# Performance work log

Measured on AMD Instinct MI355X. Metric: run time of the kernel, lower is better.

## Reference

```python
import jax, jax.numpy as jnp
import numpy as np

WS, OWS, NH = 16, 24, 2          # window size, overlap window size (=int(16*0.5)+16), num heads
PAD = (OWS - WS) // 2            # unfold padding = 4


def conv2d(x, w, b):
    kh, kw = w.shape[2], w.shape[3]
    out = jax.lax.conv_general_dilated(x, w, (1, 1), [(kh // 2, kh // 2), (kw // 2, kw // 2)],
                                       dimension_numbers=('NCHW', 'OIHW', 'NCHW'))
    return out + b[None, :, None, None]


def layer_norm(x, g, b, eps=1e-5):
    m = x.mean(-1, keepdims=True)
    v = ((x - m) ** 2).mean(-1, keepdims=True)
    return (x - m) * jax.lax.rsqrt(v + eps) * g + b


def stem(depth, cw1, cb1, cw2, cb2, cw3, cb3, cw4, cb4, in_g, in_b):
    # BasicConv(1->8,k3,relu) -> (8->16,k1,relu) -> (16->16,k3,relu) -> (16->32,k1) -> InstanceNorm2d(32,affine)
    y = jax.nn.relu(conv2d(depth, cw1, cb1))
    y = jax.nn.relu(conv2d(y, cw2, cb2))
    y = jax.nn.relu(conv2d(y, cw3, cb3))
    y = conv2d(y, cw4, cb4)
    m = y.mean((2, 3), keepdims=True)
    v = ((y - m) ** 2).mean((2, 3), keepdims=True)
    return (y - m) * jax.lax.rsqrt(v + 1e-5) * in_g[None, :, None, None] + in_b[None, :, None, None]


def ocab(xq, ykv, rpi, n1g, n1b, wq, bq, wkv, bkv, rpb, wp, bp, n2g, n2b, mw1, mb1, mw2, mb2):
    # Overlapping cross-attention block (HAT-style OCAB, cross variant: q from xq, kv from ykv).
    b, c, h, w = xq.shape
    x = xq.transpose(0, 2, 3, 1)   # b h w c
    y = ykv.transpose(0, 2, 3, 1)
    shortcut = x
    q = layer_norm(x, n1g, n1b) @ wq + bq          # b h w c
    kv = layer_norm(y, n1g, n1b) @ wkv + bkv       # b h w 2c
    nhw, nww = h // WS, w // WS
    # non-overlapping query windows: (b*nw, WS*WS, c)
    qw = q.reshape(b, nhw, WS, nww, WS, c).transpose(0, 1, 3, 2, 4, 5).reshape(b * nhw * nww, WS * WS, c)
    # overlapping kv windows via unfold (patch channel order = (channel, kh, kw), same as torch unfold)
    patches = jax.lax.conv_general_dilated_patches(kv.transpose(0, 3, 1, 2), (OWS, OWS), (WS, WS),
                                                   [(PAD, PAD), (PAD, PAD)])  # b, 2c*OWS*OWS, nhw, nww
    patches = patches.reshape(b, 2, c, OWS * OWS, nhw * nww).transpose(1, 0, 4, 3, 2).reshape(2, b * nhw * nww, OWS * OWS, c)
    k, v = patches[0], patches[1]
    d = c // NH
    qh = qw.reshape(-1, WS * WS, NH, d).transpose(0, 2, 1, 3) * (d ** -0.5)
    kh = k.reshape(-1, OWS * OWS, NH, d).transpose(0, 2, 1, 3)
    vh = v.reshape(-1, OWS * OWS, NH, d).transpose(0, 2, 1, 3)
    attn = jnp.einsum('whqd,whkd->whqk', qh, kh)
    attn = attn + rpb[rpi].transpose(2, 0, 1)[None]  # rel-pos bias -> [1, NH, WS*WS, OWS*OWS]
    attn = jax.nn.softmax(attn, axis=-1)
    out = jnp.einsum('whqk,whkd->whqd', attn, vh).transpose(0, 2, 1, 3).reshape(-1, WS * WS, c)
    # window reverse
    out = out.reshape(b, nhw, nww, WS, WS, c).transpose(0, 1, 3, 2, 4, 5).reshape(b, h, w, c)
    out = out @ wp + bp + shortcut
    out = out + (jax.nn.gelu(layer_norm(out, n2g, n2b) @ mw1 + mb1) @ mw2 + mb2)  # mlp_ratio=2
    return out.transpose(0, 3, 1, 2)


def setup_inputs():
    key = jax.random.key(0)
    ks = jax.random.split(key, 16)
    B, C, H, W = 1, 32, 256, 256
    s = 0.05
    return dict(
        x=jax.random.normal(ks[0], (B, C, H, W), jnp.float32),
        depth=jax.random.normal(ks[1], (B, 1, H, W), jnp.float32),
        rpi=jax.random.randint(ks[2], (WS * WS, OWS * OWS), 0, (WS + OWS - 1) ** 2),
        cw1=jax.random.normal(ks[3], (8, 1, 3, 3)) * s, cb1=jnp.zeros(8),
        cw2=jax.random.normal(ks[4], (16, 8, 1, 1)) * s, cb2=jnp.zeros(16),
        cw3=jax.random.normal(ks[5], (16, 16, 3, 3)) * s, cb3=jnp.zeros(16),
        cw4=jax.random.normal(ks[6], (32, 16, 1, 1)) * s, cb4=jnp.zeros(32),
        in_g=jnp.ones(32), in_b=jnp.zeros(32),
        n1g=jnp.ones(C), n1b=jnp.zeros(C),
        wq=jax.random.normal(ks[7], (C, C)) * s, bq=jnp.zeros(C),
        wkv=jax.random.normal(ks[8], (C, 2 * C)) * s, bkv=jnp.zeros(2 * C),
        rpb=jax.random.normal(ks[9], ((WS + OWS - 1) ** 2, NH)) * 0.02,
        wp=jax.random.normal(ks[10], (C, C)) * s, bp=jnp.zeros(C),
        n2g=jnp.ones(C), n2b=jnp.zeros(C),
        mw1=jax.random.normal(ks[11], (C, 2 * C)) * s, mb1=jnp.zeros(2 * C),
        mw2=jax.random.normal(ks[12], (2 * C, C)) * s, mb2=jnp.zeros(C),
    )


def reference(x, depth, rpi, cw1, cb1, cw2, cb2, cw3, cb3, cw4, cb4, in_g, in_b,
              n1g, n1b, wq, bq, wkv, bkv, rpb, wp, bp, n2g, n2b, mw1, mb1, mw2, mb2):
    f = stem(depth, cw1, cb1, cw2, cb2, cw3, cb3, cw4, cb4, in_g, in_b)
    a = (n1g, n1b, wq, bq, wkv, bkv, rpb, wp, bp, n2g, n2b, mw1, mb1, mw2, mb2)
    out1 = ocab(x, f, rpi, *a)   # shared OCAB weights, called twice with swapped roles
    out2 = ocab(f, x, rpi, *a)
    return out1 + out2 + x
```

## Files before the change

### kernel.cpp

```cpp
#include <hip/hip_runtime.h>
#include <hip/hip_bf16.h>

#define HW 65536
#define KPAD 584

typedef __attribute__((ext_vector_type(8))) short bf8;
typedef __attribute__((ext_vector_type(4))) float f4;

__device__ __forceinline__ unsigned short f2b(float x) {
  unsigned int u = __float_as_uint(x);
  unsigned int r = (u + 0x7fff + ((u >> 16) & 1)) >> 16;
  return (unsigned short)r;
}
__device__ __forceinline__ unsigned int pk2(float lo, float hi) {
  return (__float_as_uint(hi) & 0xffff0000u) | (__float_as_uint(lo) >> 16);
}
__device__ __forceinline__ float ex2(float x) { return __builtin_amdgcn_exp2f(x); }

__device__ __forceinline__ void stem_front_body(
    int bx, int t, const float* __restrict__ depth,
    const float* __restrict__ cw1, const float* __restrict__ cb1,
    const float* __restrict__ cw2, const float* __restrict__ cb2,
    float* __restrict__ t2) {
  int p = bx * 256 + t;
  int y = p >> 8, x = p & 255;
  float in9[9];
#pragma unroll
  for (int ky = 0; ky < 3; ky++)
#pragma unroll
    for (int kx = 0; kx < 3; kx++) {
      int yy = y + ky - 1, xx = x + kx - 1;
      bool ok = ((unsigned)yy < 256u) && ((unsigned)xx < 256u);
      in9[ky*3+kx] = ok ? depth[yy*256+xx] : 0.f;
    }
  float t1[8];
#pragma unroll
  for (int o = 0; o < 8; o++) {
    float s = cb1[o];
#pragma unroll
    for (int i = 0; i < 9; i++) s += in9[i] * cw1[o*9+i];
    t1[o] = fmaxf(s, 0.f);
  }
#pragma unroll
  for (int o = 0; o < 16; o++) {
    float s = cb2[o];
#pragma unroll
    for (int ci = 0; ci < 8; ci++) s += t1[ci] * cw2[o*8+ci];
    t2[o*HW + p] = fmaxf(s, 0.f);
  }
}

__device__ __forceinline__ void bias_body(
    int bx, int t, const int* __restrict__ rpi,
    const float* __restrict__ rpb, float* __restrict__ biasT) {
  int idx = bx*256 + t;
  int hd = idx / 147456;
  int rem = idx - hd*147456;
  int qt = rem / 9216;
  int r2 = rem - qt*9216;
  int kb = r2 >> 6;
  int q16 = (r2 >> 2) & 15;
  int r = r2 & 3;
  int key = kb*4 + r;
  int qq = qt*16 + q16;
  biasT[idx] = (rpb[rpi[qq*576 + key]*2 + hd] - 8.0f) * 1.44269504f;
}

__device__ __forceinline__ void lnmm16_body(
    int role, int bx, int t,
    float* ws, float* gs, float* bs, float* b2s, float* as, float* bbs,
    const float* __restrict__ x, const float* __restrict__ t4,
    const float* __restrict__ part,
    const float* __restrict__ ig, const float* __restrict__ ib,
    const float* __restrict__ n1g, const float* __restrict__ n1b,
    const float* __restrict__ wq, const float* __restrict__ bq,
    const float* __restrict__ wkv, const float* __restrict__ bkv,
    float* q1, float* kv1, float* q2, float* kv2) {
  const float *src, *wm, *bo; float* dst;
  int wstride, wcol; bool ain;
  if (role < 6) { src = x;  ain = false; } else { src = t4; ain = true; }
  switch (role) {
    default:
    case 0:  wm=wq;  wstride=32; wcol=0;  bo=bq;  dst=q1;               break;
    case 1:  wm=wq;  wstride=32; wcol=16; bo=bq;  dst=q1+16*HW;         break;
    case 2: case 3: case 4: case 5:
             wm=wkv; wstride=64; wcol=16*(role-2); bo=bkv; dst=kv2+16*(role-2)*HW; break;
    case 6:  wm=wq;  wstride=32; wcol=0;  bo=bq;  dst=q2;               break;
    case 7:  wm=wq;  wstride=32; wcol=16; bo=bq;  dst=q2+16*HW;         break;
    case 8: case 9: case 10: case 11:
             wm=wkv; wstride=64; wcol=16*(role-8); bo=bkv; dst=kv1+16*(role-8)*HW; break;
  }
  for (int i = t; i < 512; i += 256) ws[i] = wm[(i>>4)*wstride + wcol + (i&15)];
  if (t < 16) b2s[t] = bo[wcol + t];
  if (t < 32) {
    gs[t] = n1g[t]; bs[t] = n1b[t];
    if (ain) {
      float s = 0.f, ss = 0.f;
#pragma unroll
      for (int k = 0; k < 16; k++) { s += part[t*16+k]; ss += part[512 + t*16+k]; }
      float m = s * (1.f/65536.f);
      float var = ss * (1.f/65536.f) - m*m;
      float a = rsqrtf(var + 1e-5f) * ig[t];
      as[t] = a; bbs[t] = ib[t] - m*a;
    }
  }
  __syncthreads();
  int p = bx*256 + t;
  float v[32]; float s = 0.f;
  if (ain) {
#pragma unroll
    for (int c = 0; c < 32; c++) { v[c] = src[c*HW+p]*as[c] + bbs[c]; s += v[c]; }
  } else {
#pragma unroll
    for (int c = 0; c < 32; c++) { v[c] = src[c*HW+p]; s += v[c]; }
  }
  float m = s * 0.03125f;
  float ss = 0.f;
#pragma unroll
  for (int c = 0; c < 32; c++) { float d = v[c]-m; ss += d*d; }
  float rs = rsqrtf(ss*0.03125f + 1e-5f);
  float acc[16];
#pragma unroll
  for (int j = 0; j < 16; j++) acc[j] = b2s[j];
#pragma unroll
  for (int c = 0; c < 32; c++) {
    float ln = (v[c]-m)*rs*gs[c] + bs[c];
    const float4* w4 = (const float4*)&ws[c*16];
#pragma unroll
    for (int j4 = 0; j4 < 4; j4++) {
      float4 w = w4[j4];
      acc[j4*4+0] += ln*w.x; acc[j4*4+1] += ln*w.y;
      acc[j4*4+2] += ln*w.z; acc[j4*4+3] += ln*w.w;
    }
  }
#pragma unroll
  for (int j = 0; j < 16; j++) dst[j*HW+p] = acc[j];
}

__global__ __launch_bounds__(256) void k_misc(
    const float* __restrict__ depth,
    const float* __restrict__ cw1, const float* __restrict__ cb1,
    const float* __restrict__ cw2, const float* __restrict__ cb2,
    float* __restrict__ t2,
    const int* __restrict__ rpi, const float* __restrict__ rpb, float* __restrict__ biasT,
    const float* __restrict__ x, const float* __restrict__ t4, const float* __restrict__ part,
    const float* __restrict__ ig, const float* __restrict__ ib,
    const float* __restrict__ n1g, const float* __restrict__ n1b,
    const float* __restrict__ wq, const float* __restrict__ bq,
    const float* __restrict__ wkv, const float* __restrict__ bkv,
    float* q1, float* kv1, float* q2, float* kv2) {
  __shared__ __align__(16) float ws[512];
  __shared__ float gs[32], bs[32], b2s[16], as[32], bbs[32];
  int id = blockIdx.x, t = threadIdx.x;
  if (id < 256) { stem_front_body(id, t, depth, cw1, cb1, cw2, cb2, t2); return; }
  if (id < 1408) { bias_body(id - 256, t, rpi, rpb, biasT); return; }
  int r = id - 1408;
  lnmm16_body(r >> 8, r & 255, t, ws, gs, bs, b2s, as, bbs,
              x, t4, part, ig, ib, n1g, n1b, wq, bq, wkv, bkv, q1, kv1, q2, kv2);
}

__global__ __launch_bounds__(256) void k_lnmmB(
    const float* __restrict__ x, const float* __restrict__ t4, const float* __restrict__ part,
    const float* __restrict__ ig, const float* __restrict__ ib,
    const float* __restrict__ n1g, const float* __restrict__ n1b,
    const float* __restrict__ wq, const float* __restrict__ bq,
    const float* __restrict__ wkv, const float* __restrict__ bkv,
    float* q1, float* kv1, float* q2, float* kv2, int ybase) {
  __shared__ __align__(16) float ws[512];
  __shared__ float gs[32], bs[32], b2s[16], as[32], bbs[32];
  lnmm16_body(ybase + blockIdx.y, blockIdx.x, threadIdx.x, ws, gs, bs, b2s, as, bbs,
              x, t4, part, ig, ib, n1g, n1b, wq, bq, wkv, bkv, q1, kv1, q2, kv2);
}

__global__ __launch_bounds__(256) void k_conv3(
    const float* __restrict__ t2, const float* __restrict__ cw3,
    const float* __restrict__ cb3, float* __restrict__ t3) {
  int t = threadIdx.x;
  int p = blockIdx.x*256 + t;
  int og = blockIdx.y;
  int y = p >> 8, x = p & 255;
  float acc[4];
#pragma unroll
  for (int o = 0; o < 4; o++) acc[o] = cb3[og*4+o];
#pragma unroll 1
  for (int tap = 0; tap < 9; tap++) {
    int ky = tap/3 - 1, kx = tap - (tap/3)*3 - 1;
    int yy = y+ky, xx = x+kx;
    bool ok = ((unsigned)yy < 256u) && ((unsigned)xx < 256u);
    int pp = yy*256+xx;
#pragma unroll
    for (int ci = 0; ci < 16; ci++) {
      float v = ok ? t2[ci*HW+pp] : 0.f;
#pragma unroll
      for (int o = 0; o < 4; o++)
        acc[o] += v * cw3[(og*4+o)*144 + ci*9 + tap];
    }
  }
#pragma unroll
  for (int o = 0; o < 4; o++) t3[(og*4+o)*HW+p] = fmaxf(acc[o], 0.f);
}

__global__ __launch_bounds__(256) void k_conv4(
    const float* __restrict__ t3, const float* __restrict__ cw4,
    const float* __restrict__ cb4, float* __restrict__ t4) {
  int t = threadIdx.x;
  int p = blockIdx.x*256 + t;
  int og = blockIdx.y;
  float v[16];
#pragma unroll
  for (int ci = 0; ci < 16; ci++) v[ci] = t3[ci*HW+p];
#pragma unroll
  for (int o = 0; o < 8; o++) {
    int oo = og*8 + o;
    float s = cb4[oo];
#pragma unroll
    for (int ci = 0; ci < 16; ci++) s += v[ci]*cw4[oo*16+ci];
    t4[oo*HW+p] = s;
  }
}

__global__ __launch_bounds__(256) void k_instats1(const float* __restrict__ t4,
                                                  float* __restrict__ part) {
  int c = blockIdx.x >> 4, seg = blockIdx.x & 15;
  const float4* src = (const float4*)(t4 + c*HW + seg*4096);
  float s = 0.f, ss = 0.f;
  for (int i = threadIdx.x; i < 1024; i += 256) {
    float4 v = src[i];
    s  += v.x + v.y + v.z + v.w;
    ss += v.x*v.x + v.y*v.y + v.z*v.z + v.w*v.w;
  }
#pragma unroll
  for (int off = 32; off > 0; off >>= 1) {
    s  += __shfl_down(s, off, 64);
    ss += __shfl_down(ss, off, 64);
  }
  __shared__ float sh[8];
  int wid = threadIdx.x >> 6;
  if ((threadIdx.x & 63) == 0) { sh[wid] = s; sh[4+wid] = ss; }
  __syncthreads();
  if (threadIdx.x == 0) {
    part[blockIdx.x]       = sh[0]+sh[1]+sh[2]+sh[3];
    part[512 + blockIdx.x] = sh[4]+sh[5]+sh[6]+sh[7];
  }
}

__global__ __launch_bounds__(256, 4) void k_attn(
    const float* __restrict__ qA, const float* __restrict__ kvA, float* __restrict__ aoA,
    const float* __restrict__ qB, const float* __restrict__ kvB, float* __restrict__ aoB,
    const float* __restrict__ biasT) {
  __shared__ __align__(16) unsigned short Ks[576*16];
  __shared__ __align__(16) unsigned short Vt[16*KPAD];

  const float* q  = blockIdx.y ? qB  : qA;
  const float* kv = blockIdx.y ? kvB : kvA;
  float* ao       = blockIdx.y ? aoB : aoA;

  int id = blockIdx.x;
  int lin = ((id & 7) << 6) | (id >> 3);
  int wi = lin >> 1, hd = lin & 1;
  int wy = wi >> 4, wx = wi & 15;
  int t = threadIdx.x;
  int by = wy*16 - 4, bx = wx*16 - 4;
  int kbase = hd*16*HW, vbase = (32 + hd*16)*HW;

  int wave = t >> 6, lane = t & 63;
  int quad = lane >> 4, l16 = lane & 15;
  const bf8 zero8 = {0,0,0,0,0,0,0,0};

  bf8 qf[4];
#pragma unroll
  for (int qi = 0; qi < 4; qi++) {
    int qt = wave*4 + qi;
    if (quad < 2) {
      int prow = (wy*16 + qt)*256 + wx*16 + l16;
      unsigned short qtmp[8];
#pragma unroll
      for (int j = 0; j < 8; j++)
        qtmp[j] = f2b(q[(hd*16 + quad*8 + j)*HW + prow] * 0.360673503f);
      qf[qi] = *(const bf8*)qtmp;
    } else {
      qf[qi] = zero8;
    }
  }

  for (int e = t; e < 576; e += 256) {
    int dy = e / 24, dx = e - dy*24;
    int yy = by + dy, xx = bx + dx;
    bool ok = ((unsigned)yy < 256u) && ((unsigned)xx < 256u);
    int pp = yy*256 + xx;
    int off = e & 31;
    int ppos = ((off & 12) << 1) + ((off >> 4) << 2) + (off & 3);
    int vcol = (e & ~31) + ppos;
    unsigned short tk[16];
#pragma unroll
    for (int i = 0; i < 16; i++) {
      float kvl = ok ? kv[kbase + i*HW + pp] : 0.f;
      float vvl = ok ? kv[vbase + i*HW + pp] : 0.f;
      tk[i] = f2b(kvl);
      Vt[i*KPAD + vcol] = f2b(vvl);
    }
    *(uint4*)&Ks[e*16]     = *(uint4*)&tk[0];
    *(uint4*)&Ks[e*16 + 8] = *(uint4*)&tk[8];
  }
  __syncthreads();

  f4 oacc[4];
  float lr[4];
  const float* bb[4];
#pragma unroll
  for (int qi = 0; qi < 4; qi++) {
    int qt = wave*4 + qi;
    oacc[qi] = (f4){0.f,0.f,0.f,0.f};
    lr[qi] = 0.f;
    bb[qi] = biasT + (hd*16 + qt)*9216 + quad*64 + l16*4;
  }

#pragma unroll 2
  for (int kt2 = 0; kt2 < 18; kt2++) {
    int k0 = kt2 * 32;
    bf8 kf0 = zero8, kf1 = zero8;
    if (quad < 2) {
      kf0 = *(const bf8*)&Ks[(k0 + l16)*16 + quad*8];
      kf1 = *(const bf8*)&Ks[(k0 + 16 + l16)*16 + quad*8];
    }
    bf8 vf = *(const bf8*)&Vt[l16*KPAD + k0 + quad*8];
#pragma unroll
    for (int qi = 0; qi < 4; qi++) {
      f4 b0 = *(const f4*)&bb[qi][k0*16];
      f4 b1 = *(const f4*)&bb[qi][(k0+16)*16];
      f4 s0 = __builtin_amdgcn_mfma_f32_16x16x32_bf16(kf0, qf[qi], b0, 0, 0, 0);
      f4 s1 = __builtin_amdgcn_mfma_f32_16x16x32_bf16(kf1, qf[qi], b1, 0, 0, 0);
      float p0[4], p1[4];
#pragma unroll
      for (int r = 0; r < 4; r++) {
        p0[r] = ex2(s0[r]);
        p1[r] = ex2(s1[r]);
        lr[qi] += p0[r] + p1[r];
      }
      union { unsigned int u[4]; bf8 v; } P;
      P.u[0] = pk2(p0[0], p0[1]); P.u[1] = pk2(p0[2], p0[3]);
      P.u[2] = pk2(p1[0], p1[1]); P.u[3] = pk2(p1[2], p1[3]);
      oacc[qi] = __builtin_amdgcn_mfma_f32_16x16x32_bf16(P.v, vf, oacc[qi], 0, 0, 0);
    }
  }
#pragma unroll
  for (int qi = 0; qi < 4; qi++) {
    lr[qi] += __shfl_xor(lr[qi], 16, 64);
    lr[qi] += __shfl_xor(lr[qi], 32, 64);
  }
#pragma unroll
  for (int qi = 0; qi < 4; qi++) {
    int qt = wave*4 + qi;
#pragma unroll
    for (int r = 0; r < 4; r++) {
      float lv = __shfl(lr[qi], quad*4 + r, 64);
      int qw = qt*16 + quad*4 + r;
      ao[(hd*16 + l16)*HW + (wy*16 + (qw >> 4))*256 + wx*16 + (qw & 15)] = oacc[qi][r] / lv;
    }
  }
}

__global__ __launch_bounds__(256) void k_projmlp(
    const float* __restrict__ ao1, const float* __restrict__ ao2,
    const float* __restrict__ x, const float* __restrict__ t4,
    const float* __restrict__ part,
    const float* __restrict__ ig, const float* __restrict__ ib,
    const float* __restrict__ wp, const float* __restrict__ bp,
    const float* __restrict__ n2g, const float* __restrict__ n2b,
    const float* __restrict__ mw1, const float* __restrict__ mb1,
    const float* __restrict__ mw2, const float* __restrict__ mb2,
    float* __restrict__ o1, float* __restrict__ o2, int obase) {
  int oc = blockIdx.y + obase;
  const float* ao = oc ? ao2 : ao1;
  float* dst      = oc ? o2  : o1;
  __shared__ __align__(16) float wps[1024];
  __shared__ __align__(16) float w1s[2048];
  __shared__ __align__(16) float w2s[2048];
  __shared__ float bps[32], b1s[64], b2s[32], gs[32], bs[32], as[32], bbs[32];
  int t = threadIdx.x;
  for (int i = t; i < 1024; i += 256) wps[i] = wp[i];
  for (int i = t; i < 2048; i += 256) { w1s[i] = mw1[i]; w2s[i] = mw2[i]; }
  if (t < 64) b1s[t] = mb1[t];
  if (t < 32) {
    bps[t] = bp[t]; b2s[t] = mb2[t]; gs[t] = n2g[t]; bs[t] = n2b[t];
    float s = 0.f, ss = 0.f;
#pragma unroll
    for (int k = 0; k < 16; k++) { s += part[t*16+k]; ss += part[512 + t*16+k]; }
    float m = s * (1.f/65536.f);
    float var = ss * (1.f/65536.f) - m*m;
    float a = rsqrtf(var + 1e-5f) * ig[t];
    as[t] = a; bbs[t] = ib[t] - m*a;
  }
  __syncthreads();
  int p = blockIdx.x*256 + t;
  float acc[32];
#pragma unroll
  for (int j = 0; j < 32; j++) acc[j] = bps[j];
#pragma unroll
  for (int c = 0; c < 32; c++) {
    float vc = ao[c*HW+p];
    const float4* w4 = (const float4*)&wps[c*32];
#pragma unroll
    for (int j4 = 0; j4 < 8; j4++) {
      float4 w = w4[j4];
      acc[j4*4+0] += vc*w.x; acc[j4*4+1] += vc*w.y;
      acc[j4*4+2] += vc*w.z; acc[j4*4+3] += vc*w.w;
    }
  }
  if (oc == 0) {
#pragma unroll
    for (int j = 0; j < 32; j++) acc[j] += x[j*HW+p];
  } else {
#pragma unroll
    for (int j = 0; j < 32; j++) acc[j] += t4[j*HW+p]*as[j] + bbs[j];
  }
  float s = 0.f;
#pragma unroll
  for (int j = 0; j < 32; j++) s += acc[j];
  float m = s * 0.03125f;
  float ss = 0.f;
#pragma unroll
  for (int j = 0; j < 32; j++) { float d = acc[j]-m; ss += d*d; }
  float rs = rsqrtf(ss*0.03125f + 1e-5f);
  float r[32];
#pragma unroll
  for (int j = 0; j < 32; j++) r[j] = b2s[j];
#pragma unroll 1
  for (int half = 0; half < 2; half++) {
    float h[32];
#pragma unroll
    for (int k = 0; k < 32; k++) h[k] = b1s[half*32 + k];
#pragma unroll
    for (int c = 0; c < 32; c++) {
      float ln = (acc[c] - m) * rs * gs[c] + bs[c];
      const float4* w4 = (const float4*)&w1s[c*64 + half*32];
#pragma unroll
      for (int k4 = 0; k4 < 8; k4++) {
        float4 w = w4[k4];
        h[k4*4+0] += ln*w.x; h[k4*4+1] += ln*w.y; h[k4*4+2] += ln*w.z; h[k4*4+3] += ln*w.w;
      }
    }
#pragma unroll
    for (int k = 0; k < 32; k++) {
      float xx = h[k];
      float u = 0.7978845608f * (xx + 0.044715f*xx*xx*xx);
      float th = 1.f - 2.f/(1.f + __expf(2.f*u));
      h[k] = 0.5f * xx * (1.f + th);
    }
#pragma unroll
    for (int k = 0; k < 32; k++) {
      float hk = h[k];
      const float4* w4 = (const float4*)&w2s[(half*32 + k)*32];
#pragma unroll
      for (int j4 = 0; j4 < 8; j4++) {
        float4 w = w4[j4];
        r[j4*4+0] += hk*w.x; r[j4*4+1] += hk*w.y; r[j4*4+2] += hk*w.z; r[j4*4+3] += hk*w.w;
      }
    }
  }
#pragma unroll
  for (int j = 0; j < 32; j++) dst[j*HW + p] = acc[j] + r[j];
}

__global__ __launch_bounds__(256) void k_final(
    const float* o1, const float* __restrict__ o2,
    const float* __restrict__ x, float* out) {
  int i = blockIdx.x*256 + threadIdx.x;
  float4 a = ((const float4*)o1)[i];
  float4 b = ((const float4*)o2)[i];
  float4 c = ((const float4*)x)[i];
  float4 r;
  r.x = a.x + b.x + c.x; r.y = a.y + b.y + c.y;
  r.z = a.z + b.z + c.z; r.w = a.w + b.w + c.w;
  ((float4*)out)[i] = r;
}

extern "C" void kernel_launch(void* const* d_in, const int* in_sizes, int n_in,
                              void* d_out, int out_size, void* d_ws, size_t ws_size,
                              hipStream_t stream) {
  const float* x    = (const float*)d_in[0];
  const float* depth= (const float*)d_in[1];
  const int*   rpi  = (const int*)d_in[2];
  const float* cw1  = (const float*)d_in[3],  *cb1 = (const float*)d_in[4];
  const float* cw2  = (const float*)d_in[5],  *cb2 = (const float*)d_in[6];
  const float* cw3  = (const float*)d_in[7],  *cb3 = (const float*)d_in[8];
  const float* cw4  = (const float*)d_in[9],  *cb4 = (const float*)d_in[10];
  const float* in_g = (const float*)d_in[11], *in_b = (const float*)d_in[12];
  const float* n1g  = (const float*)d_in[13], *n1b = (const float*)d_in[14];
  const float* wq   = (const float*)d_in[15], *bq  = (const float*)d_in[16];
  const float* wkv  = (const float*)d_in[17], *bkv = (const float*)d_in[18];
  const float* rpb  = (const float*)d_in[19];
  const float* wp   = (const float*)d_in[20], *bp  = (const float*)d_in[21];
  const float* n2g  = (const float*)d_in[22], *n2b = (const float*)d_in[23];
  const float* mw1  = (const float*)d_in[24], *mb1 = (const float*)d_in[25];
  const float* mw2  = (const float*)d_in[26], *mb2 = (const float*)d_in[27];

  float* W   = (float*)d_ws;
  float* o1  = (float*)d_out;

  bool big = ws_size >= (size_t)85100000;

  if (big) {
    float* t4    = W;
    float* q1    = W + 2097152;
    float* q2    = W + 4194304;
    float* kv1   = W + 6291456;
    float* kv2   = W + 10485760;
    float* ao1   = W + 14680064;
    float* ao2   = W + 16777216;
    float* o2    = W + 18874368;
    float* biasT = W + 20971520;
    float* part  = W + 21266432;
    float* t2 = ao1, *t3 = q2;

    k_misc   <<<2944, 256, 0, stream>>>(depth, cw1, cb1, cw2, cb2, t2,
                                        rpi, rpb, biasT,
                                        x, t4, part, in_g, in_b, n1g, n1b,
                                        wq, bq, wkv, bkv, q1, kv1, q2, kv2);
    k_conv3  <<<dim3(256,4), 256, 0, stream>>>(t2, cw3, cb3, t3);
    k_conv4  <<<dim3(256,4), 256, 0, stream>>>(t3, cw4, cb4, t4);
    k_instats1<<<512, 256, 0, stream>>>(t4, part);
    k_lnmmB  <<<dim3(256,6), 256, 0, stream>>>(x, t4, part, in_g, in_b, n1g, n1b,
                                               wq, bq, wkv, bkv, q1, kv1, q2, kv2, 6);
    k_attn   <<<dim3(512,2), 256, 0, stream>>>(q1, kv1, ao1, q2, kv2, ao2, biasT);
    k_projmlp<<<dim3(256,2), 256, 0, stream>>>(ao1, ao2, x, t4, part, in_g, in_b,
                                               wp, bp, n2g, n2b, mw1, mb1, mw2, mb2,
                                               o1, o2, 0);
    k_final  <<<2048, 256, 0, stream>>>(o1, o2, x, o1);
  } else {
    float* t4    = W;
    float* q1    = W + 2097152;
    float* kv1   = W + 4194304;
    float* ao1   = W + 8388608;
    float* o2    = W + 10485760;
    float* biasT = W + 12582912;
    float* part  = W + 12877824;
    float* t2 = ao1, *t3 = o2;

    k_misc   <<<1920, 256, 0, stream>>>(depth, cw1, cb1, cw2, cb2, t2,
                                        rpi, rpb, biasT,
                                        x, t4, part, in_g, in_b, n1g, n1b,
                                        wq, bq, wkv, bkv, q1, kv1, q1, kv1);
    k_conv3  <<<dim3(256,4), 256, 0, stream>>>(t2, cw3, cb3, t3);
    k_conv4  <<<dim3(256,4), 256, 0, stream>>>(t3, cw4, cb4, t4);
    k_instats1<<<512, 256, 0, stream>>>(t4, part);
    k_lnmmB  <<<dim3(256,4), 256, 0, stream>>>(x, t4, part, in_g, in_b, n1g, n1b,
                                               wq, bq, wkv, bkv, q1, kv1, q1, kv1, 8);
    k_attn   <<<dim3(512,1), 256, 0, stream>>>(q1, kv1, ao1, q1, kv1, ao1, biasT);
    k_projmlp<<<dim3(256,1), 256, 0, stream>>>(ao1, ao1, x, t4, part, in_g, in_b,
                                               wp, bp, n2g, n2b, mw1, mb1, mw2, mb2,
                                               o1, o2, 0);
    k_lnmmB  <<<dim3(256,6), 256, 0, stream>>>(x, t4, part, in_g, in_b, n1g, n1b,
                                               wq, bq, wkv, bkv, q1, kv1, q1, kv1, 2);
    k_attn   <<<dim3(512,1), 256, 0, stream>>>(q1, kv1, ao1, q1, kv1, ao1, biasT);
    k_projmlp<<<dim3(256,1), 256, 0, stream>>>(ao1, ao1, x, t4, part, in_g, in_b,
                                               wp, bp, n2g, n2b, mw1, mb1, mw2, mb2,
                                               o1, o2, 1);
    k_final  <<<2048, 256, 0, stream>>>(o1, o2, x, o1);
  }
}
```

Before: 261.7 us.

## Split attention KV into halves, pack bias to bf16, widen LN-projection outputs

Attention now runs each window as two half-KV blocks (split-K) with smaller shared memory and higher occupancy, writing unnormalized bf16 partial outputs and row sums that the projection/MLP kernel combines and normalizes. The relative-position bias table is packed into bf16 pairs to halve its traffic. The LN+QKV projection computes 48 outputs per thread instead of 16, so each input is normalized once per slice rather than six times. Weights in proj/MLP are read directly from global instead of staged in LDS, and the small-workspace fallback path is removed. These changes add bf16 rounding of partial attention outputs and sums, and the fixed max-shift of 8 is dropped from the bias, which risks exp overflow for large logits.

```diff
diff --git a/kernel.cpp b/kernel.cpp
--- a/kernel.cpp
+++ b/kernel.cpp
@@ -2,7 +2,8 @@
 #include <hip/hip_bf16.h>
 
 #define HW 65536
-#define KPAD 584
+#define KHALF 288
+#define KPAD2 328
 
 typedef __attribute__((ext_vector_type(8))) short bf8;
 typedef __attribute__((ext_vector_type(4))) float f4;
@@ -14,6 +15,9 @@
 }
 __device__ __forceinline__ unsigned int pk2(float lo, float hi) {
   return (__float_as_uint(hi) & 0xffff0000u) | (__float_as_uint(lo) >> 16);
+}
+__device__ __forceinline__ float b2f(unsigned short u) {
+  return __uint_as_float(((unsigned int)u) << 16);
 }
 __device__ __forceinline__ float ex2(float x) { return __builtin_amdgcn_exp2f(x); }
 
@@ -50,25 +54,104 @@
   }
 }
 
-__device__ __forceinline__ void bias_body(
+__device__ __forceinline__ void bias_pk_body(
     int bx, int t, const int* __restrict__ rpi,
-    const float* __restrict__ rpb, float* __restrict__ biasT) {
+    const float* __restrict__ rpb, unsigned int* __restrict__ biasPk) {
   int idx = bx*256 + t;
-  int hd = idx / 147456;
-  int rem = idx - hd*147456;
-  int qt = rem / 9216;
-  int r2 = rem - qt*9216;
-  int kb = r2 >> 6;
-  int q16 = (r2 >> 2) & 15;
-  int r = r2 & 3;
-  int key = kb*4 + r;
-  int qq = qt*16 + q16;
-  biasT[idx] = (rpb[rpi[qq*576 + key]*2 + hd] - 8.0f) * 1.44269504f;
-}
-
-__device__ __forceinline__ void lnmm16_body(
-    int role, int bx, int t,
-    float* ws, float* gs, float* bs, float* b2s, float* as, float* bbs,
+  int hd = idx / 73728;
+  int rem = idx - hd*73728;
+  int qt = rem / 4608;
+  int r2 = rem - qt*4608;
+  int kt2 = r2 >> 8;
+  int w8 = r2 & 255;
+  int quad = w8 >> 6, q = (w8 >> 2) & 15, r = w8 & 3;
+  int klo = kt2*32 + quad*4 + r;
+  int qq = qt*16 + q;
+  float lo = rpb[rpi[qq*576 + klo]*2 + hd] * 1.44269504f;
+  float hi = rpb[rpi[qq*576 + klo + 16]*2 + hd] * 1.44269504f;
+  biasPk[idx] = ((unsigned int)f2b(hi) << 16) | (unsigned int)f2b(lo);
+}
+
+__device__ __forceinline__ void lnmm48_body(
+    int role, int bx, int t, float* as_, float* bbs_,
+    const float* __restrict__ x, const float* __restrict__ t4,
+    const float* __restrict__ part,
+    const float* __restrict__ ig, const float* __restrict__ ib,
+    const float* __restrict__ n1g, const float* __restrict__ n1b,
+    const float* __restrict__ wq, const float* __restrict__ bq,
+    const float* __restrict__ wkv, const float* __restrict__ bkv,
+    float* __restrict__ q1, float* __restrict__ kv1,
+    float* __restrict__ q2, float* __restrict__ kv2) {
+  bool ain = role >= 2;
+  int slice = role & 1;
+  const float* src = ain ? t4 : x;
+  float* dq  = ain ? q2 : q1;
+  float* dkv = ain ? kv1 : kv2;
+  if (ain) {
+    if (t < 32) {
+      float s = 0.f, ss = 0.f;
+#pragma unroll
+      for (int k = 0; k < 16; k++) { s += part[t*16+k]; ss += part[512 + t*16+k]; }
+      float m = s * (1.f/65536.f);
+      float var = ss * (1.f/65536.f) - m*m;
+      float a = rsqrtf(var + 1e-5f) * ig[t];
+      as_[t] = a; bbs_[t] = ib[t] - m*a;
+    }
+    __syncthreads();
+  }
+  int p = bx*256 + t;
+  float v[32]; float s = 0.f;
+  if (ain) {
+#pragma unroll
+    for (int c = 0; c < 32; c++) { v[c] = src[c*HW+p]*as_[c] + bbs_[c]; s += v[c]; }
+  } else {
+#pragma unroll
+    for (int c = 0; c < 32; c++) { v[c] = src[c*HW+p]; s += v[c]; }
+  }
+  float m = s * 0.03125f;
+  float ss = 0.f;
+#pragma unroll
+  for (int c = 0; c < 32; c++) { float d = v[c]-m; ss += d*d; }
+  float rs = rsqrtf(ss*0.03125f + 1e-5f);
+  float acc[48];
+  if (slice == 0) {
+#pragma unroll
+    for (int j = 0; j < 32; j++) acc[j] = bq[j];
+#pragma unroll
+    for (int j = 0; j < 16; j++) acc[32+j] = bkv[j];
+#pragma unroll
+    for (int c = 0; c < 32; c++) {
+      float ln = (v[c]-m)*rs*n1g[c] + n1b[c];
+#pragma unroll
+      for (int j = 0; j < 32; j++) acc[j] += ln*wq[c*32+j];
+#pragma unroll
+      for (int j = 0; j < 16; j++) acc[32+j] += ln*wkv[c*64+j];
+    }
+#pragma unroll
+    for (int j = 0; j < 32; j++) dq[j*HW+p] = acc[j];
+#pragma unroll
+    for (int j = 0; j < 16; j++) dkv[j*HW+p] = acc[32+j];
+  } else {
+#pragma unroll
+    for (int j = 0; j < 48; j++) acc[j] = bkv[16+j];
+#pragma unroll
+    for (int c = 0; c < 32; c++) {
+      float ln = (v[c]-m)*rs*n1g[c] + n1b[c];
+#pragma unroll
+      for (int j = 0; j < 48; j++) acc[j] += ln*wkv[c*64+16+j];
+    }
+#pragma unroll
+    for (int j = 0; j < 48; j++) dkv[(16+j)*HW+p] = acc[j];
+  }
+}
+
+__global__ __launch_bounds__(256, 2) void k_misc(
+    const float* __restrict__ depth,
+    const float* __restrict__ cw1, const float* __restrict__ cb1,
+    const float* __restrict__ cw2, const float* __restrict__ cb2,
+    float* __restrict__ t2,
+    const int* __restrict__ rpi, const float* __restrict__ rpb,
+    unsigned int* __restrict__ biasPk,
     const float* __restrict__ x, const float* __restrict__ t4,
     const float* __restrict__ part,
     const float* __restrict__ ig, const float* __restrict__ ib,
@@ -76,99 +159,25 @@
     const float* __restrict__ wq, const float* __restrict__ bq,
     const float* __restrict__ wkv, const float* __restrict__ bkv,
     float* q1, float* kv1, float* q2, float* kv2) {
-  const float *src, *wm, *bo; float* dst;
-  int wstride, wcol; bool ain;
-  if (role < 6) { src = x;  ain = false; } else { src = t4; ain = true; }
-  switch (role) {
-    default:
-    case 0:  wm=wq;  wstride=32; wcol=0;  bo=bq;  dst=q1;               break;
-    case 1:  wm=wq;  wstride=32; wcol=16; bo=bq;  dst=q1+16*HW;         break;
-    case 2: case 3: case 4: case 5:
-             wm=wkv; wstride=64; wcol=16*(role-2); bo=bkv; dst=kv2+16*(role-2)*HW; break;
-    case 6:  wm=wq;  wstride=32; wcol=0;  bo=bq;  dst=q2;               break;
-    case 7:  wm=wq;  wstride=32; wcol=16; bo=bq;  dst=q2+16*HW;         break;
-    case 8: case 9: case 10: case 11:
-             wm=wkv; wstride=64; wcol=16*(role-8); bo=bkv; dst=kv1+16*(role-8)*HW; break;
-  }
-  for (int i = t; i < 512; i += 256) ws[i] = wm[(i>>4)*wstride + wcol + (i&15)];
-  if (t < 16) b2s[t] = bo[wcol + t];
-  if (t < 32) {
-    gs[t] = n1g[t]; bs[t] = n1b[t];
-    if (ain) {
-      float s = 0.f, ss = 0.f;
-#pragma unroll
-      for (int k = 0; k < 16; k++) { s += part[t*16+k]; ss += part[512 + t*16+k]; }
-      float m = s * (1.f/65536.f);
-      float var = ss * (1.f/65536.f) - m*m;
-      float a = rsqrtf(var + 1e-5f) * ig[t];
-      as[t] = a; bbs[t] = ib[t] - m*a;
-    }
-  }
-  __syncthreads();
-  int p = bx*256 + t;
-  float v[32]; float s = 0.f;
-  if (ain) {
-#pragma unroll
-    for (int c = 0; c < 32; c++) { v[c] = src[c*HW+p]*as[c] + bbs[c]; s += v[c]; }
-  } else {
-#pragma unroll
-    for (int c = 0; c < 32; c++) { v[c] = src[c*HW+p]; s += v[c]; }
-  }
-  float m = s * 0.03125f;
-  float ss = 0.f;
-#pragma unroll
-  for (int c = 0; c < 32; c++) { float d = v[c]-m; ss += d*d; }
-  float rs = rsqrtf(ss*0.03125f + 1e-5f);
-  float acc[16];
-#pragma unroll
-  for (int j = 0; j < 16; j++) acc[j] = b2s[j];
-#pragma unroll
-  for (int c = 0; c < 32; c++) {
-    float ln = (v[c]-m)*rs*gs[c] + bs[c];
-    const float4* w4 = (const float4*)&ws[c*16];
-#pragma unroll
-    for (int j4 = 0; j4 < 4; j4++) {
-      float4 w = w4[j4];
-      acc[j4*4+0] += ln*w.x; acc[j4*4+1] += ln*w.y;
-      acc[j4*4+2] += ln*w.z; acc[j4*4+3] += ln*w.w;
-    }
-  }
-#pragma unroll
-  for (int j = 0; j < 16; j++) dst[j*HW+p] = acc[j];
-}
-
-__global__ __launch_bounds__(256) void k_misc(
-    const float* __restrict__ depth,
-    const float* __restrict__ cw1, const float* __restrict__ cb1,
-    const float* __restrict__ cw2, const float* __restrict__ cb2,
-    float* __restrict__ t2,
-    const int* __restrict__ rpi, const float* __restrict__ rpb, float* __restrict__ biasT,
-    const float* __restrict__ x, const float* __restrict__ t4, const float* __restrict__ part,
+  __shared__ float as_[32], bbs_[32];
+  int id = blockIdx.x, t = threadIdx.x;
+  if (id < 256) { stem_front_body(id, t, depth, cw1, cb1, cw2, cb2, t2); return; }
+  if (id < 832) { bias_pk_body(id - 256, t, rpi, rpb, biasPk); return; }
+  int r = id - 832;
+  lnmm48_body(r >> 8, r & 255, t, as_, bbs_,
+              x, t4, part, ig, ib, n1g, n1b, wq, bq, wkv, bkv, q1, kv1, q2, kv2);
+}
+
+__global__ __launch_bounds__(256, 2) void k_lnmmB2(
+    const float* __restrict__ x, const float* __restrict__ t4,
+    const float* __restrict__ part,
     const float* __restrict__ ig, const float* __restrict__ ib,
     const float* __restrict__ n1g, const float* __restrict__ n1b,
     const float* __restrict__ wq, const float* __restrict__ bq,
     const float* __restrict__ wkv, const float* __restrict__ bkv,
     float* q1, float* kv1, float* q2, float* kv2) {
-  __shared__ __align__(16) float ws[512];
-  __shared__ float gs[32], bs[32], b2s[16], as[32], bbs[32];
-  int id = blockIdx.x, t = threadIdx.x;
-  if (id < 256) { stem_front_body(id, t, depth, cw1, cb1, cw2, cb2, t2); return; }
-  if (id < 1408) { bias_body(id - 256, t, rpi, rpb, biasT); return; }
-  int r = id - 1408;
-  lnmm16_body(r >> 8, r & 255, t, ws, gs, bs, b2s, as, bbs,
-              x, t4, part, ig, ib, n1g, n1b, wq, bq, wkv, bkv, q1, kv1, q2, kv2);
-}
-
-__global__ __launch_bounds__(256) void k_lnmmB(
-    const float* __restrict__ x, const float* __restrict__ t4, const float* __restrict__ part,
-    const float* __restrict__ ig, const float* __restrict__ ib,
-    const float* __restrict__ n1g, const float* __restrict__ n1b,
-    const float* __restrict__ wq, const float* __restrict__ bq,
-    const float* __restrict__ wkv, const float* __restrict__ bkv,
-    float* q1, float* kv1, float* q2, float* kv2, int ybase) {
-  __shared__ __align__(16) float ws[512];
-  __shared__ float gs[32], bs[32], b2s[16], as[32], bbs[32];
-  lnmm16_body(ybase + blockIdx.y, blockIdx.x, threadIdx.x, ws, gs, bs, b2s, as, bbs,
+  __shared__ float as_[32], bbs_[32];
+  lnmm48_body(2 + blockIdx.y, blockIdx.x, threadIdx.x, as_, bbs_,
               x, t4, part, ig, ib, n1g, n1b, wq, bq, wkv, bkv, q1, kv1, q2, kv2);
 }
 
@@ -244,23 +253,27 @@
   }
 }
 
-__global__ __launch_bounds__(256, 4) void k_attn(
-    const float* __restrict__ qA, const float* __restrict__ kvA, float* __restrict__ aoA,
-    const float* __restrict__ qB, const float* __restrict__ kvB, float* __restrict__ aoB,
-    const float* __restrict__ biasT) {
-  __shared__ __align__(16) unsigned short Ks[576*16];
-  __shared__ __align__(16) unsigned short Vt[16*KPAD];
-
-  const float* q  = blockIdx.y ? qB  : qA;
-  const float* kv = blockIdx.y ? kvB : kvA;
-  float* ao       = blockIdx.y ? aoB : aoA;
+__global__ __launch_bounds__(256, 8) void k_attn(
+    const float* __restrict__ qA, const float* __restrict__ kvA,
+    unsigned short* __restrict__ paoA, unsigned short* __restrict__ plA,
+    const float* __restrict__ qB, const float* __restrict__ kvB,
+    unsigned short* __restrict__ paoB, unsigned short* __restrict__ plB,
+    const unsigned int* __restrict__ biasPk) {
+  __shared__ __align__(16) unsigned short Ks[KHALF*16];
+  __shared__ __align__(16) unsigned short Vt[16*KPAD2];
+
+  int sel = blockIdx.y >> 1, half = blockIdx.y & 1;
+  const float* q  = sel ? qB  : qA;
+  const float* kv = sel ? kvB : kvA;
+  unsigned short* pao = sel ? paoB : paoA;
+  unsigned short* pl  = sel ? plB  : plA;
 
   int id = blockIdx.x;
   int lin = ((id & 7) << 6) | (id >> 3);
   int wi = lin >> 1, hd = lin & 1;
   int wy = wi >> 4, wx = wi & 15;
   int t = threadIdx.x;
-  int by = wy*16 - 4, bx = wx*16 - 4;
+  int by = wy*16 - 4 + half*12, bx = wx*16 - 4;
   int kbase = hd*16*HW, vbase = (32 + hd*16)*HW;
 
   int wave = t >> 6, lane = t & 63;
@@ -283,7 +296,7 @@
     }
   }
 
-  for (int e = t; e < 576; e += 256) {
+  for (int e = t; e < KHALF; e += 256) {
     int dy = e / 24, dx = e - dy*24;
     int yy = by + dy, xx = bx + dx;
     bool ok = ((unsigned)yy < 256u) && ((unsigned)xx < 256u);
@@ -297,7 +310,7 @@
       float kvl = ok ? kv[kbase + i*HW + pp] : 0.f;
       float vvl = ok ? kv[vbase + i*HW + pp] : 0.f;
       tk[i] = f2b(kvl);
-      Vt[i*KPAD + vcol] = f2b(vvl);
+      Vt[i*KPAD2 + vcol] = f2b(vvl);
     }
     *(uint4*)&Ks[e*16]     = *(uint4*)&tk[0];
     *(uint4*)&Ks[e*16 + 8] = *(uint4*)&tk[8];
@@ -306,28 +319,36 @@
 
   f4 oacc[4];
   float lr[4];
-  const float* bb[4];
+  unsigned int bboff[4];
 #pragma unroll
   for (int qi = 0; qi < 4; qi++) {
     int qt = wave*4 + qi;
     oacc[qi] = (f4){0.f,0.f,0.f,0.f};
     lr[qi] = 0.f;
-    bb[qi] = biasT + (hd*16 + qt)*9216 + quad*64 + l16*4;
+    bboff[qi] = (unsigned)((hd*16 + qt)*4608 + half*2304 + quad*64 + l16*4);
   }
 
 #pragma unroll 2
-  for (int kt2 = 0; kt2 < 18; kt2++) {
+  for (int kt2 = 0; kt2 < 9; kt2++) {
     int k0 = kt2 * 32;
     bf8 kf0 = zero8, kf1 = zero8;
     if (quad < 2) {
       kf0 = *(const bf8*)&Ks[(k0 + l16)*16 + quad*8];
       kf1 = *(const bf8*)&Ks[(k0 + 16 + l16)*16 + quad*8];
     }
-    bf8 vf = *(const bf8*)&Vt[l16*KPAD + k0 + quad*8];
+    bf8 vf = *(const bf8*)&Vt[l16*KPAD2 + k0 + quad*8];
+    __builtin_amdgcn_s_setprio(1);
 #pragma unroll
     for (int qi = 0; qi < 4; qi++) {
-      f4 b0 = *(const f4*)&bb[qi][k0*16];
-      f4 b1 = *(const f4*)&bb[qi][(k0+16)*16];
+      union { uint4 v; unsigned int u[4]; } bw;
+      bw.v = *(const uint4*)&biasPk[bboff[qi] + kt2*256];
+      f4 b0, b1;
+#pragma unroll
+      for (int r = 0; r < 4; r++) {
+        unsigned int u = bw.u[r];
+        b0[r] = __uint_as_float(u << 16);
+        b1[r] = __uint_as_float(u & 0xffff0000u);
+      }
       f4 s0 = __builtin_amdgcn_mfma_f32_16x16x32_bf16(kf0, qf[qi], b0, 0, 0, 0);
       f4 s1 = __builtin_amdgcn_mfma_f32_16x16x32_bf16(kf1, qf[qi], b1, 0, 0, 0);
       float p0[4], p1[4];
@@ -342,6 +363,7 @@
       P.u[2] = pk2(p1[0], p1[1]); P.u[3] = pk2(p1[2], p1[3]);
       oacc[qi] = __builtin_amdgcn_mfma_f32_16x16x32_bf16(P.v, vf, oacc[qi], 0, 0, 0);
     }
+    __builtin_amdgcn_s_setprio(0);
   }
 #pragma unroll
   for (int qi = 0; qi < 4; qi++) {
@@ -353,15 +375,18 @@
     int qt = wave*4 + qi;
 #pragma unroll
     for (int r = 0; r < 4; r++) {
-      float lv = __shfl(lr[qi], quad*4 + r, 64);
-      int qw = qt*16 + quad*4 + r;
-      ao[(hd*16 + l16)*HW + (wy*16 + (qw >> 4))*256 + wx*16 + (qw & 15)] = oacc[qi][r] / lv;
+      int col = quad*4 + r;
+      pao[(half*32 + hd*16 + l16)*HW + (wy*16 + qt)*256 + wx*16 + col] = f2b(oacc[qi][r]);
+    }
+    if (quad == 0) {
+      pl[(half*2 + hd)*HW + (wy*16 + qt)*256 + wx*16 + l16] = f2b(lr[qi]);
     }
   }
 }
 
 __global__ __launch_bounds__(256) void k_projmlp(
-    const float* __restrict__ ao1, const float* __restrict__ ao2,
+    const unsigned short* __restrict__ pao1, const unsigned short* __restrict__ pl1,
+    const unsigned short* __restrict__ pao2, const unsigned short* __restrict__ pl2,
     const float* __restrict__ x, const float* __restrict__ t4,
     const float* __restrict__ part,
     const float* __restrict__ ig, const float* __restrict__ ib,
@@ -369,50 +394,41 @@
     const float* __restrict__ n2g, const float* __restrict__ n2b,
     const float* __restrict__ mw1, const float* __restrict__ mb1,
     const float* __restrict__ mw2, const float* __restrict__ mb2,
-    float* __restrict__ o1, float* __restrict__ o2, int obase) {
-  int oc = blockIdx.y + obase;
-  const float* ao = oc ? ao2 : ao1;
-  float* dst      = oc ? o2  : o1;
-  __shared__ __align__(16) float wps[1024];
-  __shared__ __align__(16) float w1s[2048];
-  __shared__ __align__(16) float w2s[2048];
-  __shared__ float bps[32], b1s[64], b2s[32], gs[32], bs[32], as[32], bbs[32];
+    float* __restrict__ o1, float* __restrict__ o2) {
+  int oc = blockIdx.y;
+  const unsigned short* pao = oc ? pao2 : pao1;
+  const unsigned short* pl  = oc ? pl2  : pl1;
+  float* dst = oc ? o2 : o1;
+  __shared__ float as_[32], bbs_[32];
   int t = threadIdx.x;
-  for (int i = t; i < 1024; i += 256) wps[i] = wp[i];
-  for (int i = t; i < 2048; i += 256) { w1s[i] = mw1[i]; w2s[i] = mw2[i]; }
-  if (t < 64) b1s[t] = mb1[t];
   if (t < 32) {
-    bps[t] = bp[t]; b2s[t] = mb2[t]; gs[t] = n2g[t]; bs[t] = n2b[t];
     float s = 0.f, ss = 0.f;
 #pragma unroll
     for (int k = 0; k < 16; k++) { s += part[t*16+k]; ss += part[512 + t*16+k]; }
     float m = s * (1.f/65536.f);
     float var = ss * (1.f/65536.f) - m*m;
     float a = rsqrtf(var + 1e-5f) * ig[t];
-    as[t] = a; bbs[t] = ib[t] - m*a;
+    as_[t] = a; bbs_[t] = ib[t] - m*a;
   }
   __syncthreads();
   int p = blockIdx.x*256 + t;
+  float inv0 = 1.f / (b2f(pl[p])      + b2f(pl[2*HW+p]));
+  float inv1 = 1.f / (b2f(pl[HW+p])   + b2f(pl[3*HW+p]));
   float acc[32];
 #pragma unroll
-  for (int j = 0; j < 32; j++) acc[j] = bps[j];
+  for (int j = 0; j < 32; j++) acc[j] = bp[j];
 #pragma unroll
   for (int c = 0; c < 32; c++) {
-    float vc = ao[c*HW+p];
-    const float4* w4 = (const float4*)&wps[c*32];
-#pragma unroll
-    for (int j4 = 0; j4 < 8; j4++) {
-      float4 w = w4[j4];
-      acc[j4*4+0] += vc*w.x; acc[j4*4+1] += vc*w.y;
-      acc[j4*4+2] += vc*w.z; acc[j4*4+3] += vc*w.w;
-    }
+    float vc = (b2f(pao[c*HW+p]) + b2f(pao[(32+c)*HW+p])) * (c < 16 ? inv0 : inv1);
+#pragma unroll
+    for (int j = 0; j < 32; j++) acc[j] += vc * wp[c*32+j];
   }
   if (oc == 0) {
 #pragma unroll
     for (int j = 0; j < 32; j++) acc[j] += x[j*HW+p];
   } else {
 #pragma unroll
-    for (int j = 0; j < 32; j++) acc[j] += t4[j*HW+p]*as[j] + bbs[j];
+    for (int j = 0; j < 32; j++) acc[j] += t4[j*HW+p]*as_[j] + bbs_[j];
   }
   float s = 0.f;
 #pragma unroll
@@ -424,21 +440,17 @@
   float rs = rsqrtf(ss*0.03125f + 1e-5f);
   float r[32];
 #pragma unroll
-  for (int j = 0; j < 32; j++) r[j] = b2s[j];
+  for (int j = 0; j < 32; j++) r[j] = mb2[j];
 #pragma unroll 1
   for (int half = 0; half < 2; half++) {
     float h[32];
 #pragma unroll
-    for (int k = 0; k < 32; k++) h[k] = b1s[half*32 + k];
+    for (int k = 0; k < 32; k++) h[k] = mb1[half*32 + k];
 #pragma unroll
     for (int c = 0; c < 32; c++) {
-      float ln = (acc[c] - m) * rs * gs[c] + bs[c];
-      const float4* w4 = (const float4*)&w1s[c*64 + half*32];
-#pragma unroll
-      for (int k4 = 0; k4 < 8; k4++) {
-        float4 w = w4[k4];
-        h[k4*4+0] += ln*w.x; h[k4*4+1] += ln*w.y; h[k4*4+2] += ln*w.z; h[k4*4+3] += ln*w.w;
-      }
+      float ln = (acc[c] - m) * rs * n2g[c] + n2b[c];
+#pragma unroll
+      for (int k = 0; k < 32; k++) h[k] += ln * mw1[c*64 + half*32 + k];
     }
 #pragma unroll
     for (int k = 0; k < 32; k++) {
@@ -450,12 +462,8 @@
 #pragma unroll
     for (int k = 0; k < 32; k++) {
       float hk = h[k];
-      const float4* w4 = (const float4*)&w2s[(half*32 + k)*32];
-#pragma unroll
-      for (int j4 = 0; j4 < 8; j4++) {
-        float4 w = w4[j4];
-        r[j4*4+0] += hk*w.x; r[j4*4+1] += hk*w.y; r[j4*4+2] += hk*w.z; r[j4*4+3] += hk*w.w;
-      }
+#pragma unroll
+      for (int j = 0; j < 32; j++) r[j] += hk * mw2[(half*32 + k)*32 + j];
     }
   }
 #pragma unroll
@@ -498,64 +506,34 @@
   float* W   = (float*)d_ws;
   float* o1  = (float*)d_out;
 
-  bool big = ws_size >= (size_t)85100000;
-
-  if (big) {
-    float* t4    = W;
-    float* q1    = W + 2097152;
-    float* q2    = W + 4194304;
-    float* kv1   = W + 6291456;
-    float* kv2   = W + 10485760;
-    float* ao1   = W + 14680064;
-    float* ao2   = W + 16777216;
-    float* o2    = W + 18874368;
-    float* biasT = W + 20971520;
-    float* part  = W + 21266432;
-    float* t2 = ao1, *t3 = q2;
-
-    k_misc   <<<2944, 256, 0, stream>>>(depth, cw1, cb1, cw2, cb2, t2,
-                                        rpi, rpb, biasT,
-                                        x, t4, part, in_g, in_b, n1g, n1b,
-                                        wq, bq, wkv, bkv, q1, kv1, q2, kv2);
-    k_conv3  <<<dim3(256,4), 256, 0, stream>>>(t2, cw3, cb3, t3);
-    k_conv4  <<<dim3(256,4), 256, 0, stream>>>(t3, cw4, cb4, t4);
-    k_instats1<<<512, 256, 0, stream>>>(t4, part);
-    k_lnmmB  <<<dim3(256,6), 256, 0, stream>>>(x, t4, part, in_g, in_b, n1g, n1b,
-                                               wq, bq, wkv, bkv, q1, kv1, q2, kv2, 6);
-    k_attn   <<<dim3(512,2), 256, 0, stream>>>(q1, kv1, ao1, q2, kv2, ao2, biasT);
-    k_projmlp<<<dim3(256,2), 256, 0, stream>>>(ao1, ao2, x, t4, part, in_g, in_b,
-                                               wp, bp, n2g, n2b, mw1, mb1, mw2, mb2,
-                                               o1, o2, 0);
-    k_final  <<<2048, 256, 0, stream>>>(o1, o2, x, o1);
-  } else {
-    float* t4    = W;
-    float* q1    = W + 2097152;
-    float* kv1   = W + 4194304;
-    float* ao1   = W + 8388608;
-    float* o2    = W + 10485760;
-    float* biasT = W + 12582912;
-    float* part  = W + 12877824;
-    float* t2 = ao1, *t3 = o2;
-
-    k_misc   <<<1920, 256, 0, stream>>>(depth, cw1, cb1, cw2, cb2, t2,
-                                        rpi, rpb, biasT,
-                                        x, t4, part, in_g, in_b, n1g, n1b,
-                                        wq, bq, wkv, bkv, q1, kv1, q1, kv1);
-    k_conv3  <<<dim3(256,4), 256, 0, stream>>>(t2, cw3, cb3, t3);
-    k_conv4  <<<dim3(256,4), 256, 0, stream>>>(t3, cw4, cb4, t4);
-    k_instats1<<<512, 256, 0, stream>>>(t4, part);
-    k_lnmmB  <<<dim3(256,4), 256, 0, stream>>>(x, t4, part, in_g, in_b, n1g, n1b,
-                                               wq, bq, wkv, bkv, q1, kv1, q1, kv1, 8);
-    k_attn   <<<dim3(512,1), 256, 0, stream>>>(q1, kv1, ao1, q1, kv1, ao1, biasT);
-    k_projmlp<<<dim3(256,1), 256, 0, stream>>>(ao1, ao1, x, t4, part, in_g, in_b,
-                                               wp, bp, n2g, n2b, mw1, mb1, mw2, mb2,
-                                               o1, o2, 0);
-    k_lnmmB  <<<dim3(256,6), 256, 0, stream>>>(x, t4, part, in_g, in_b, n1g, n1b,
-                                               wq, bq, wkv, bkv, q1, kv1, q1, kv1, 2);
-    k_attn   <<<dim3(512,1), 256, 0, stream>>>(q1, kv1, ao1, q1, kv1, ao1, biasT);
-    k_projmlp<<<dim3(256,1), 256, 0, stream>>>(ao1, ao1, x, t4, part, in_g, in_b,
-                                               wp, bp, n2g, n2b, mw1, mb1, mw2, mb2,
-                                               o1, o2, 1);
-    k_final  <<<2048, 256, 0, stream>>>(o1, o2, x, o1);
-  }
-}
+  float* t4    = W;
+  float* q1    = W + 2097152;
+  float* q2    = W + 4194304;
+  float* kv1   = W + 6291456;
+  float* kv2   = W + 10485760;
+  unsigned short* pao1 = (unsigned short*)(W + 14680064);
+  unsigned short* pao2 = (unsigned short*)(W + 16777216);
+  unsigned short* pl1  = (unsigned short*)(W + 18874368);
+  unsigned short* pl2  = (unsigned short*)(W + 19005440);
+  unsigned int* biasPk = (unsigned int*)(W + 19136512);
+  float* part  = W + 19283968;
+  float* t2 = (float*)pao1;
+  float* t3 = q2;
+  float* o2 = q1;
+
+  k_misc   <<<1344, 256, 0, stream>>>(depth, cw1, cb1, cw2, cb2, t2,
+                                      rpi, rpb, biasPk,
+                                      x, t4, part, in_g, in_b, n1g, n1b,
+                                      wq, bq, wkv, bkv, q1, kv1, q2, kv2);
+  k_conv3  <<<dim3(256,4), 256, 0, stream>>>(t2, cw3, cb3, t3);
+  k_conv4  <<<dim3(256,4), 256, 0, stream>>>(t3, cw4, cb4, t4);
+  k_instats1<<<512, 256, 0, stream>>>(t4, part);
+  k_lnmmB2 <<<dim3(256,2), 256, 0, stream>>>(x, t4, part, in_g, in_b, n1g, n1b,
+                                             wq, bq, wkv, bkv, q1, kv1, q2, kv2);
+  k_attn   <<<dim3(512,4), 256, 0, stream>>>(q1, kv1, pao1, pl1,
+                                             q2, kv2, pao2, pl2, biasPk);
+  k_projmlp<<<dim3(256,2), 256, 0, stream>>>(pao1, pl1, pao2, pl2, x, t4, part,
+                                             in_g, in_b, wp, bp, n2g, n2b,
+                                             mw1, mb1, mw2, mb2, o1, o2);
+  k_final  <<<2048, 256, 0, stream>>>(o1, o2, x, o1);
+}
```

Measured after the change: 619.8 us. 137% more time.
